# Kernel optimization log

Measured on AMD Instinct MI355X. Metric: run time of the kernel, lower is better.

Reference implementation:

```python
import jax, jax.numpy as jnp
import numpy as np

N, M, D = 8192, 8192, 64


def _ball_points(key, n, d, r_lo=0.1, r_hi=0.85):
    k1, k2 = jax.random.split(key)
    v = jax.random.normal(k1, (n, d), dtype=jnp.float32)
    v = v / jnp.linalg.norm(v, axis=1, keepdims=True)
    r = jax.random.uniform(k2, (n, 1), dtype=jnp.float32, minval=r_lo, maxval=r_hi)
    return v * r  # points strictly inside the unit ball


def setup_inputs() -> dict:
    key = jax.random.key(0)
    ka, kb = jax.random.split(key)
    a = _ball_points(ka, N, D)
    b = _ball_points(kb, M, D)
    return {"a": a, "b": b}


def reference(a, b):
    # squared norms [N], [M]
    a2 = jnp.sum(a * a, axis=1)
    b2 = jnp.sum(b * b, axis=1)
    # pairwise Euclidean distance via GEMM trick: ||a||^2 + ||b||^2 - 2 a.b
    sq = a2[:, None] + b2[None, :] - 2.0 * (a @ b.T)  # [N, M]
    d = jnp.sqrt(jnp.maximum(sq, 0.0))
    # Poincare-style scaling (note: module uses distance d, not d^2)
    denom = (1.0 - a2)[:, None] * (1.0 - b2)[None, :]  # [N, M]
    inner = 1.0 + 2.0 * d / denom
    # arcosh(x) = log(x + sqrt(x^2 - 1))
    return jnp.log(inner + jnp.sqrt(inner * inner - 1.0))
```

## Files before the change

kernel.cpp:

```cpp
#include <hip/hip_runtime.h>

typedef unsigned short ushort_t;
typedef short bf16x8 __attribute__((ext_vector_type(8)));
typedef float f32x4 __attribute__((ext_vector_type(4)));

#define NPTS 8192
#define DIM 64

__global__ __launch_bounds__(256) void prep_kernel(
    const float* __restrict__ src, ushort_t* __restrict__ hi,
    ushort_t* __restrict__ lo, float* __restrict__ s2,
    float* __restrict__ iv, float scale)
{
    int idx = blockIdx.x * 256 + threadIdx.x;
    float v = src[idx];
    unsigned u = __float_as_uint(v);
    unsigned hb = (u + 0x7fffu + ((u >> 16) & 1u)) >> 16;
    float hf = __uint_as_float(hb << 16);
    float l = v - hf;
    unsigned ul = __float_as_uint(l);
    unsigned lb = (ul + 0x7fffu + ((ul >> 16) & 1u)) >> 16;
    hi[idx] = (ushort_t)hb;
    lo[idx] = (ushort_t)lb;
    float p = v * v;
    #pragma unroll
    for (int m = 1; m < 64; m <<= 1) p += __shfl_xor(p, m, 64);
    if ((threadIdx.x & 63) == 0) {
        int row = idx >> 6;
        s2[row] = p;
        iv[row] = scale / (1.0f - p);
    }
}

__global__ __launch_bounds__(256) void poincare_kernel(
    const ushort_t* __restrict__ ahi, const ushort_t* __restrict__ alo,
    const ushort_t* __restrict__ bhi, const ushort_t* __restrict__ blo,
    const float* __restrict__ a2v, const float* __restrict__ iva,
    const float* __restrict__ b2v, const float* __restrict__ ivb,
    float* __restrict__ out)
{
    int lane = threadIdx.x & 63;
    int wid  = threadIdx.x >> 6;
    int bx = blockIdx.x & (NPTS / 128 - 1);
    int by = blockIdx.x / (NPTS / 128);
    int row0 = by * 128 + (wid >> 1) * 64;
    int col0 = bx * 128 + (wid & 1) * 64;
    int r16 = lane & 15;
    int kq  = lane >> 4;

    bf16x8 bfh[4][2], bfl[4][2];
    #pragma unroll
    for (int cb = 0; cb < 4; ++cb)
        #pragma unroll
        for (int ks = 0; ks < 2; ++ks) {
            int off = (col0 + cb * 16 + r16) * DIM + ks * 32 + kq * 8;
            bfh[cb][ks] = *(const bf16x8*)(bhi + off);
            bfl[cb][ks] = *(const bf16x8*)(blo + off);
        }

    f32x4 acc[4][4];
    #pragma unroll
    for (int rb = 0; rb < 4; ++rb)
        #pragma unroll
        for (int cb = 0; cb < 4; ++cb)
            acc[rb][cb] = (f32x4){0.f, 0.f, 0.f, 0.f};

    #pragma unroll
    for (int rb = 0; rb < 4; ++rb) {
        bf16x8 afh[2], afl[2];
        #pragma unroll
        for (int ks = 0; ks < 2; ++ks) {
            int off = (row0 + rb * 16 + r16) * DIM + ks * 32 + kq * 8;
            afh[ks] = *(const bf16x8*)(ahi + off);
            afl[ks] = *(const bf16x8*)(alo + off);
        }
        #pragma unroll
        for (int cb = 0; cb < 4; ++cb) {
            f32x4 c = acc[rb][cb];
            #pragma unroll
            for (int ks = 0; ks < 2; ++ks) {
                c = __builtin_amdgcn_mfma_f32_16x16x32_bf16(afh[ks], bfh[cb][ks], c, 0, 0, 0);
                c = __builtin_amdgcn_mfma_f32_16x16x32_bf16(afh[ks], bfl[cb][ks], c, 0, 0, 0);
                c = __builtin_amdgcn_mfma_f32_16x16x32_bf16(afl[ks], bfh[cb][ks], c, 0, 0, 0);
            }
            acc[rb][cb] = c;
        }
    }

    float b2c[4], ivc[4];
    #pragma unroll
    for (int cb = 0; cb < 4; ++cb) {
        int col = col0 + cb * 16 + r16;
        b2c[cb] = b2v[col];
        ivc[cb] = ivb[col];
    }

    #pragma unroll
    for (int rb = 0; rb < 4; ++rb) {
        #pragma unroll
        for (int r = 0; r < 4; ++r) {
            int row = row0 + rb * 16 + kq * 4 + r;
            float a2r = a2v[row];
            float ivr = iva[row];
            float* orow = out + (size_t)row * NPTS + col0;
            #pragma unroll
            for (int cb = 0; cb < 4; ++cb) {
                float dot = acc[rb][cb][r];
                float sq = fmaf(-2.0f, dot, a2r + b2c[cb]);
                sq = fmaxf(sq, 0.0f);
                float d = __builtin_amdgcn_sqrtf(sq);
                float inner = fmaf(d, ivr * ivc[cb], 1.0f);
                float t = fmaf(inner, inner, -1.0f);
                t = fmaxf(t, 0.0f);
                float st = __builtin_amdgcn_sqrtf(t);
                orow[cb * 16 + r16] = __logf(inner + st);
            }
        }
    }
}

extern "C" void kernel_launch(void* const* d_in, const int* in_sizes, int n_in,
                              void* d_out, int out_size, void* d_ws, size_t ws_size,
                              hipStream_t stream)
{
    const float* a = (const float*)d_in[0];
    const float* b = (const float*)d_in[1];
    float* out = (float*)d_out;
    char* ws = (char*)d_ws;

    ushort_t* ahi = (ushort_t*)(ws);
    ushort_t* alo = (ushort_t*)(ws + (1u << 20));
    ushort_t* bhi = (ushort_t*)(ws + (2u << 20));
    ushort_t* blo = (ushort_t*)(ws + (3u << 20));
    float* a2v = (float*)(ws + (4u << 20));
    float* iva = (float*)(ws + (4u << 20) + 32768);
    float* b2v = (float*)(ws + (4u << 20) + 65536);
    float* ivb = (float*)(ws + (4u << 20) + 98304);

    prep_kernel<<<NPTS * DIM / 256, 256, 0, stream>>>(a, ahi, alo, a2v, iva, 2.0f);
    prep_kernel<<<NPTS * DIM / 256, 256, 0, stream>>>(b, bhi, blo, b2v, ivb, 1.0f);
    poincare_kernel<<<(NPTS / 128) * (NPTS / 128), 256, 0, stream>>>(
        ahi, alo, bhi, blo, a2v, iva, b2v, ivb, out);
}
```

Baseline: 304.1 us.

## Merge prep launches, shrink output tile, add occupancy hint and nontemporal stores

Fuses the two prep kernel launches into one grid that selects a or b by block index, removing one launch. The main kernel tile shrinks from 128x128 to 128x64 per block (each wave does 64x32), doubling the block count and cutting accumulator registers. A launch_bounds minimum-blocks hint of 4 is added to raise occupancy. Output writes use nontemporal stores to avoid polluting cache. The smaller tile reloads A fragments for twice as many blocks, so global A traffic goes up.

```diff
diff --git a/kernel.cpp b/kernel.cpp
--- a/kernel.cpp
+++ b/kernel.cpp
@@ -8,11 +8,21 @@
 #define DIM 64
 
 __global__ __launch_bounds__(256) void prep_kernel(
-    const float* __restrict__ src, ushort_t* __restrict__ hi,
-    ushort_t* __restrict__ lo, float* __restrict__ s2,
-    float* __restrict__ iv, float scale)
+    const float* __restrict__ a, const float* __restrict__ b,
+    ushort_t* __restrict__ ahi, ushort_t* __restrict__ alo,
+    ushort_t* __restrict__ bhi, ushort_t* __restrict__ blo,
+    float* __restrict__ a2, float* __restrict__ iva,
+    float* __restrict__ b2, float* __restrict__ ivb)
 {
-    int idx = blockIdx.x * 256 + threadIdx.x;
+    int which = blockIdx.x >> 11;
+    int idx = (blockIdx.x & 2047) * 256 + threadIdx.x;
+    const float* src = which ? b : a;
+    ushort_t* hi = which ? bhi : ahi;
+    ushort_t* lo = which ? blo : alo;
+    float* s2 = which ? b2 : a2;
+    float* iv = which ? ivb : iva;
+    float scale = which ? 1.0f : 2.0f;
+
     float v = src[idx];
     unsigned u = __float_as_uint(v);
     unsigned hb = (u + 0x7fffu + ((u >> 16) & 1u)) >> 16;
@@ -32,7 +42,7 @@
     }
 }
 
-__global__ __launch_bounds__(256) void poincare_kernel(
+__global__ __launch_bounds__(256, 4) void poincare_kernel(
     const ushort_t* __restrict__ ahi, const ushort_t* __restrict__ alo,
     const ushort_t* __restrict__ bhi, const ushort_t* __restrict__ blo,
     const float* __restrict__ a2v, const float* __restrict__ iva,
@@ -41,16 +51,16 @@
 {
     int lane = threadIdx.x & 63;
     int wid  = threadIdx.x >> 6;
-    int bx = blockIdx.x & (NPTS / 128 - 1);
-    int by = blockIdx.x / (NPTS / 128);
+    int bx = blockIdx.x & 127;
+    int by = blockIdx.x >> 7;
     int row0 = by * 128 + (wid >> 1) * 64;
-    int col0 = bx * 128 + (wid & 1) * 64;
+    int col0 = bx * 64 + (wid & 1) * 32;
     int r16 = lane & 15;
     int kq  = lane >> 4;
 
-    bf16x8 bfh[4][2], bfl[4][2];
+    bf16x8 bfh[2][2], bfl[2][2];
     #pragma unroll
-    for (int cb = 0; cb < 4; ++cb)
+    for (int cb = 0; cb < 2; ++cb)
         #pragma unroll
         for (int ks = 0; ks < 2; ++ks) {
             int off = (col0 + cb * 16 + r16) * DIM + ks * 32 + kq * 8;
@@ -58,11 +68,11 @@
             bfl[cb][ks] = *(const bf16x8*)(blo + off);
         }
 
-    f32x4 acc[4][4];
+    f32x4 acc[4][2];
     #pragma unroll
     for (int rb = 0; rb < 4; ++rb)
         #pragma unroll
-        for (int cb = 0; cb < 4; ++cb)
+        for (int cb = 0; cb < 2; ++cb)
             acc[rb][cb] = (f32x4){0.f, 0.f, 0.f, 0.f};
 
     #pragma unroll
@@ -75,7 +85,7 @@
             afl[ks] = *(const bf16x8*)(alo + off);
         }
         #pragma unroll
-        for (int cb = 0; cb < 4; ++cb) {
+        for (int cb = 0; cb < 2; ++cb) {
             f32x4 c = acc[rb][cb];
             #pragma unroll
             for (int ks = 0; ks < 2; ++ks) {
@@ -87,9 +97,9 @@
         }
     }
 
-    float b2c[4], ivc[4];
+    float b2c[2], ivc[2];
     #pragma unroll
-    for (int cb = 0; cb < 4; ++cb) {
+    for (int cb = 0; cb < 2; ++cb) {
         int col = col0 + cb * 16 + r16;
         b2c[cb] = b2v[col];
         ivc[cb] = ivb[col];
@@ -104,7 +114,7 @@
             float ivr = iva[row];
             float* orow = out + (size_t)row * NPTS + col0;
             #pragma unroll
-            for (int cb = 0; cb < 4; ++cb) {
+            for (int cb = 0; cb < 2; ++cb) {
                 float dot = acc[rb][cb][r];
                 float sq = fmaf(-2.0f, dot, a2r + b2c[cb]);
                 sq = fmaxf(sq, 0.0f);
@@ -113,7 +123,7 @@
                 float t = fmaf(inner, inner, -1.0f);
                 t = fmaxf(t, 0.0f);
                 float st = __builtin_amdgcn_sqrtf(t);
-                orow[cb * 16 + r16] = __logf(inner + st);
+                __builtin_nontemporal_store(__logf(inner + st), &orow[cb * 16 + r16]);
             }
         }
     }
@@ -137,8 +147,8 @@
     float* b2v = (float*)(ws + (4u << 20) + 65536);
     float* ivb = (float*)(ws + (4u << 20) + 98304);
 
-    prep_kernel<<<NPTS * DIM / 256, 256, 0, stream>>>(a, ahi, alo, a2v, iva, 2.0f);
-    prep_kernel<<<NPTS * DIM / 256, 256, 0, stream>>>(b, bhi, blo, b2v, ivb, 1.0f);
-    poincare_kernel<<<(NPTS / 128) * (NPTS / 128), 256, 0, stream>>>(
+    prep_kernel<<<4096, 256, 0, stream>>>(a, b, ahi, alo, bhi, blo,
+                                          a2v, iva, b2v, ivb);
+    poincare_kernel<<<128 * 64, 256, 0, stream>>>(
         ahi, alo, bhi, blo, a2v, iva, b2v, ivb, out);
 }
```

Result: slower. 332.1 us (+9.2%).
